# Optimization experiments

Measured on AMD Instinct MI355X. Metric: run time of the kernel, lower is better.

## Reference

```python
import jax, jax.numpy as jnp
import numpy as np
from jax import lax


def _box_filter(x, r):
    # depthwise (groups=ch) 2D box conv matching torch nf.conv2d(..., groups=ch)
    ch = x.shape[1]
    k = 2 * r + 1
    kernel = jnp.full((ch, 1, k, k), 1.0 / (k * k), dtype=x.dtype)
    return lax.conv_general_dilated(
        x, kernel,
        window_strides=(1, 1),
        padding=[(r, r), (r, r)],
        feature_group_count=ch,
        dimension_numbers=("NCHW", "OIHW", "NCHW"))


def setup_inputs() -> dict:
    key = jax.random.key(0)
    kx, ky = jax.random.split(key)
    B, C, H, W = 8, 3, 512, 512
    x = jax.random.uniform(kx, (B, C, H, W), dtype=jnp.float32)
    y = jax.random.uniform(ky, (B, C, H, W), dtype=jnp.float32)
    return {"x": x, "y": y, "r": 5}


def reference(x, y, r):
    eps = 0.01
    b, c, h, w = x.shape
    N = _box_filter(jnp.ones((1, 1, h, w), dtype=x.dtype), r)  # [1,1,H,W]
    mean_x = _box_filter(x, r) / N
    mean_y = _box_filter(y, r) / N
    cov_xy = _box_filter(x * y, r) / N - mean_x * mean_y
    var_x = _box_filter(x * x, r) / N - mean_x * mean_x
    A = cov_xy / (var_x + eps)
    bb = mean_y - A * mean_x
    mean_A = _box_filter(A, r) / N
    mean_b = _box_filter(bb, r) / N
    return mean_A * x + mean_b
```

## Files before the change

kernel.cpp:

```cpp
#include <hip/hip_runtime.h>


#define R    5
#define TX   64
#define TY   16
#define IMG  512
#define AROWS (TY + 2 * R)
#define ACOLS (TX + 2 * R)
#define XCOLS (TX + 4 * R)
#define V4STR 97
#define ABSTR 83
#define OFF_VAB 17280
#define SMEM_TOTAL (AROWS * V4STR * 16)

#define PB(c) ((c) + ((c) >> 3))

__device__ __forceinline__ float ccnt(int g) {
    int lo = max(g - R, 0), hi = min(g + R, IMG - 1);
    return (float)(hi - lo + 1);
}

__global__ __launch_bounds__(256, 4) void guided_fused(
        const float* __restrict__ x, const float* __restrict__ y,
        float* __restrict__ out) {
    __shared__ __align__(16) unsigned char smem[SMEM_TOTAL];
    float4 (*v4)[V4STR] = (float4(*)[V4STR])smem;
    float2 (*ab2)[ABSTR] = (float2(*)[ABSTR])smem;
    float2 (*vab)[ABSTR] = (float2(*)[ABSTR])(smem + OFF_VAB);

    const int plane = blockIdx.z;
    const int tx0 = blockIdx.x * TX;
    const int ty0 = blockIdx.y * TY;
    const int tid = threadIdx.x;
    const size_t pbase = (size_t)plane * IMG * IMG;
    const float* xp = x + pbase;
    const float* yp = y + pbase;
    const bool interior = (tx0 >= 2 * R) && (tx0 + TX + 2 * R - 1 < IMG) &&
                          (ty0 >= 2 * R) && (ty0 + TY + 2 * R - 1 < IMG);

    if (tid < 3 * XCOLS) {
        const int seg = tid / XCOLS;
        const int cc  = tid - seg * XCOLS;
        const int r0  = seg * 9;
        const int gx  = tx0 - 2 * R + cc;
        const int gy0 = ty0 - 2 * R + r0;

        float xv[19], yv[19];
        if (interior) {
            const float* xc = xp + (size_t)gy0 * IMG + gx;
            const float* yc = yp + (size_t)gy0 * IMG + gx;
#pragma unroll
            for (int j = 0; j < 19; ++j) {
                xv[j] = xc[(size_t)j * IMG];
                yv[j] = yc[(size_t)j * IMG];
            }
        } else {
            const bool xok = ((unsigned)gx < (unsigned)IMG);
#pragma unroll
            for (int j = 0; j < 19; ++j) {
                int gy = gy0 + j;
                bool ok = xok && ((unsigned)gy < (unsigned)IMG);
                size_t o = (size_t)gy * IMG + gx;
                xv[j] = ok ? xp[o] : 0.f;
                yv[j] = ok ? yp[o] : 0.f;
            }
        }
        float sx = 0.f, sy = 0.f, sxy = 0.f, sxx = 0.f;
#pragma unroll
        for (int j = 0; j < 11; ++j) {
            sx += xv[j]; sy += yv[j];
            sxy += xv[j] * yv[j]; sxx += xv[j] * xv[j];
        }
        v4[r0][PB(cc)] = make_float4(sx, sy, sxy, sxx);
#pragma unroll
        for (int s = 1; s < 9; ++s) {
            if (r0 + s < AROWS) {
                float xn = xv[s + 10], yn = yv[s + 10];
                float xo = xv[s - 1],  yo = yv[s - 1];
                sx  += xn - xo;
                sy  += yn - yo;
                sxy += xn * yn - xo * yo;
                sxx += xn * xn - xo * xo;
                v4[r0 + s][PB(cc)] = make_float4(sx, sy, sxy, sxx);
            }
        }
    }
    __syncthreads();

    int p2_r = 0, p2_c0 = 0, p2_nout = 0;
    float2 pres[10];
    if (tid < 8 * AROWS) {
        const int ch = tid / AROWS;
        const int r  = tid - ch * AROWS;
        const int c0 = 10 * ch;
        const int nout = min(10, ACOLS - c0);
        p2_r = r; p2_c0 = c0; p2_nout = nout;

        float4 ring[10];
#pragma unroll
        for (int d = 0; d < 10; ++d) ring[d] = v4[r][PB(c0 + d)];
        float sx = 0.f, sy = 0.f, sxy = 0.f, sxx = 0.f;
#pragma unroll
        for (int d = 0; d < 10; ++d) {
            sx += ring[d].x; sy += ring[d].y;
            sxy += ring[d].z; sxx += ring[d].w;
        }
        const int ay = ty0 - R + r;
        const float cy = ccnt(ay);
        const bool ayok = ((unsigned)ay < (unsigned)IMG);
#pragma unroll
        for (int i = 0; i < 10; ++i) {
            if (i < nout) {
                float4 lead = v4[r][PB(c0 + 10 + i)];
                sx += lead.x; sy += lead.y; sxy += lead.z; sxx += lead.w;
                if (i > 0) {
                    float4 o = ring[(i > 0) ? (i - 1) : 0];
                    sx -= o.x; sy -= o.y; sxy -= o.z; sxx -= o.w;
                }
                const int ac = c0 + i;
                const int ax = tx0 - R + ac;
                float A = 0.f, bb = 0.f;
                if (interior || (ayok && ((unsigned)ax < (unsigned)IMG))) {
                    float inv = interior ? (1.0f / 121.0f)
                                         : __builtin_amdgcn_rcpf(cy * ccnt(ax));
                    float mx = sx * inv, my = sy * inv;
                    float cov = sxy * inv - mx * my;
                    float var = sxx * inv - mx * mx;
                    A = cov * __builtin_amdgcn_rcpf(var + 0.01f);
                    bb = my - A * mx;
                }
                pres[i] = make_float2(A, bb);
            }
        }
    }
    __syncthreads();

    if (tid < 8 * AROWS) {
#pragma unroll
        for (int i = 0; i < 10; ++i) {
            if (i < p2_nout) ab2[p2_r][PB(p2_c0 + i)] = pres[i];
        }
    }
    __syncthreads();

    if (tid < 2 * ACOLS) {
        const int seg = (tid >= ACOLS) ? 1 : 0;
        const int ac = tid - seg * ACOLS;
        const int r0 = seg * 8;
        float2 ring[10];
#pragma unroll
        for (int d = 0; d < 10; ++d) ring[d] = ab2[r0 + d][PB(ac)];
        float sa = 0.f, sb = 0.f;
#pragma unroll
        for (int d = 0; d < 10; ++d) { sa += ring[d].x; sb += ring[d].y; }
#pragma unroll
        for (int s = 0; s < 8; ++s) {
            float2 lead = ab2[r0 + 10 + s][PB(ac)];
            sa += lead.x; sb += lead.y;
            if (s > 0) {
                float2 o = ring[(s > 0) ? (s - 1) : 0];
                sa -= o.x; sb -= o.y;
            }
            vab[r0 + s][PB(ac)] = make_float2(sa, sb);
        }
    }
    __syncthreads();

    {
        const int oy = tid >> 4;
        const int ch = tid & 15;
        const int c0 = 4 * ch;
        const int gy = ty0 + oy;
        float2 ring[10];
#pragma unroll
        for (int d = 0; d < 10; ++d) ring[d] = vab[oy][PB(c0 + d)];
        float sa = 0.f, sb = 0.f;
#pragma unroll
        for (int d = 0; d < 10; ++d) { sa += ring[d].x; sb += ring[d].y; }
        const float cy = ccnt(gy);
        const size_t obase = (size_t)gy * IMG + tx0 + c0;
        const float4 xv4 = *reinterpret_cast<const float4*>(&xp[obase]);
        const float xv[4] = {xv4.x, xv4.y, xv4.z, xv4.w};
        float res[4];
#pragma unroll
        for (int i = 0; i < 4; ++i) {
            float2 lead = vab[oy][PB(c0 + 10 + i)];
            sa += lead.x; sb += lead.y;
            if (i > 0) {
                float2 o = ring[(i > 0) ? (i - 1) : 0];
                sa -= o.x; sb -= o.y;
            }
            float inv = interior ? (1.0f / 121.0f)
                                 : __builtin_amdgcn_rcpf(cy * ccnt(tx0 + c0 + i));
            res[i] = (sa * inv) * xv[i] + (sb * inv);
        }
        *reinterpret_cast<float4*>(&out[pbase + obase]) =
            make_float4(res[0], res[1], res[2], res[3]);
    }
}

extern "C" void kernel_launch(void* const* d_in, const int* in_sizes, int n_in,
                              void* d_out, int out_size, void* d_ws, size_t ws_size,
                              hipStream_t stream) {
    const float* x = (const float*)d_in[0];
    const float* y = (const float*)d_in[1];
    float* out = (float*)d_out;

    const int planes = in_sizes[0] / (IMG * IMG);

    dim3 grid(IMG / TX, IMG / TY, planes);
    guided_fused<<<grid, 256, 0, stream>>>(x, y, out);
}
```

Measured before the change: 118.8 us.

## Rebalance horizontal passes into 8-column chunks and prefetch x before final pass

The horizontal box-sum pass now splits columns into 8-wide chunks aligned with the padding period, so shared-memory addresses become base plus constant offsets, and it uses 9 chunk threads per row instead of 8. The final output pass has 128 threads each produce 8 outputs, and the x values it needs are loaded from global memory earlier, overlapping that load with the ab2 write and the vertical pass. This aims to cut address arithmetic and hide global-load latency. In exchange, half the threads sit idle in the last pass and the per-thread serial work there doubles.

```diff
diff --git a/kernel.cpp b/kernel.cpp
--- a/kernel.cpp
+++ b/kernel.cpp
@@ -13,7 +13,8 @@
 #define OFF_VAB 17280
 #define SMEM_TOTAL (AROWS * V4STR * 16)
 
-#define PB(c) ((c) + ((c) >> 3))
+#define PB(c)   ((c) + ((c) >> 3))
+#define OFFD(d) ((d) + ((d) >> 3))
 
 __device__ __forceinline__ float ccnt(int g) {
     int lo = max(g - R, 0), hi = min(g + R, IMG - 1);
@@ -71,7 +72,8 @@
             sx += xv[j]; sy += yv[j];
             sxy += xv[j] * yv[j]; sxx += xv[j] * xv[j];
         }
-        v4[r0][PB(cc)] = make_float4(sx, sy, sxy, sxx);
+        float4* wp = &v4[r0][PB(cc)];
+        wp[0] = make_float4(sx, sy, sxy, sxx);
 #pragma unroll
         for (int s = 1; s < 9; ++s) {
             if (r0 + s < AROWS) {
@@ -81,24 +83,25 @@
                 sy  += yn - yo;
                 sxy += xn * yn - xo * yo;
                 sxx += xn * xn - xo * xo;
-                v4[r0 + s][PB(cc)] = make_float4(sx, sy, sxy, sxx);
-            }
-        }
-    }
-    __syncthreads();
-
-    int p2_r = 0, p2_c0 = 0, p2_nout = 0;
+                wp[(size_t)s * V4STR] = make_float4(sx, sy, sxy, sxx);
+            }
+        }
+    }
+    __syncthreads();
+
+    int p2_r = 0, p2_pb0 = 0, p2_nout = 0;
     float2 pres[10];
-    if (tid < 8 * AROWS) {
+    if (tid < 9 * AROWS) {
         const int ch = tid / AROWS;
         const int r  = tid - ch * AROWS;
-        const int c0 = 10 * ch;
-        const int nout = min(10, ACOLS - c0);
-        p2_r = r; p2_c0 = c0; p2_nout = nout;
-
+        const int c0 = 8 * ch;
+        const int nout = (ch == 8) ? 10 : 8;
+        p2_r = r; p2_pb0 = 9 * ch; p2_nout = nout;
+
+        const float4* bp = &v4[r][p2_pb0];
         float4 ring[10];
 #pragma unroll
-        for (int d = 0; d < 10; ++d) ring[d] = v4[r][PB(c0 + d)];
+        for (int d = 0; d < 10; ++d) ring[d] = bp[OFFD(d)];
         float sx = 0.f, sy = 0.f, sxy = 0.f, sxx = 0.f;
 #pragma unroll
         for (int d = 0; d < 10; ++d) {
@@ -111,10 +114,10 @@
 #pragma unroll
         for (int i = 0; i < 10; ++i) {
             if (i < nout) {
-                float4 lead = v4[r][PB(c0 + 10 + i)];
+                float4 lead = bp[OFFD(10 + i)];
                 sx += lead.x; sy += lead.y; sxy += lead.z; sxx += lead.w;
                 if (i > 0) {
-                    float4 o = ring[(i > 0) ? (i - 1) : 0];
+                    float4 o = ring[i - 1];
                     sx -= o.x; sy -= o.y; sxy -= o.z; sxx -= o.w;
                 }
                 const int ac = c0 + i;
@@ -135,10 +138,21 @@
     }
     __syncthreads();
 
-    if (tid < 8 * AROWS) {
+    float4 xpa = make_float4(0.f, 0.f, 0.f, 0.f), xpb = xpa;
+    size_t obase = 0;
+    if (tid < TY * 8) {
+        const int oy = tid >> 3;
+        const int ch = tid & 7;
+        obase = (size_t)(ty0 + oy) * IMG + tx0 + 8 * ch;
+        xpa = *reinterpret_cast<const float4*>(&xp[obase]);
+        xpb = *reinterpret_cast<const float4*>(&xp[obase + 4]);
+    }
+
+    if (tid < 9 * AROWS) {
+        float2* bw = &ab2[p2_r][p2_pb0];
 #pragma unroll
         for (int i = 0; i < 10; ++i) {
-            if (i < p2_nout) ab2[p2_r][PB(p2_c0 + i)] = pres[i];
+            if (i < p2_nout) bw[OFFD(i)] = pres[i];
         }
     }
     __syncthreads();
@@ -147,47 +161,49 @@
         const int seg = (tid >= ACOLS) ? 1 : 0;
         const int ac = tid - seg * ACOLS;
         const int r0 = seg * 8;
+        const float2* rp = &ab2[r0][PB(ac)];
+        float2* wp = &vab[r0][PB(ac)];
         float2 ring[10];
 #pragma unroll
-        for (int d = 0; d < 10; ++d) ring[d] = ab2[r0 + d][PB(ac)];
+        for (int d = 0; d < 10; ++d) ring[d] = rp[(size_t)d * ABSTR];
         float sa = 0.f, sb = 0.f;
 #pragma unroll
         for (int d = 0; d < 10; ++d) { sa += ring[d].x; sb += ring[d].y; }
 #pragma unroll
         for (int s = 0; s < 8; ++s) {
-            float2 lead = ab2[r0 + 10 + s][PB(ac)];
+            float2 lead = rp[(size_t)(10 + s) * ABSTR];
             sa += lead.x; sb += lead.y;
             if (s > 0) {
-                float2 o = ring[(s > 0) ? (s - 1) : 0];
+                float2 o = ring[s - 1];
                 sa -= o.x; sb -= o.y;
             }
-            vab[r0 + s][PB(ac)] = make_float2(sa, sb);
-        }
-    }
-    __syncthreads();
-
-    {
-        const int oy = tid >> 4;
-        const int ch = tid & 15;
-        const int c0 = 4 * ch;
+            wp[(size_t)s * ABSTR] = make_float2(sa, sb);
+        }
+    }
+    __syncthreads();
+
+    if (tid < TY * 8) {
+        const int oy = tid >> 3;
+        const int ch = tid & 7;
+        const int c0 = 8 * ch;
+        const float2* vb = &vab[oy][9 * ch];
+        float2 ring[10];
+#pragma unroll
+        for (int d = 0; d < 10; ++d) ring[d] = vb[OFFD(d)];
+        float sa = 0.f, sb = 0.f;
+#pragma unroll
+        for (int d = 0; d < 10; ++d) { sa += ring[d].x; sb += ring[d].y; }
         const int gy = ty0 + oy;
-        float2 ring[10];
-#pragma unroll
-        for (int d = 0; d < 10; ++d) ring[d] = vab[oy][PB(c0 + d)];
-        float sa = 0.f, sb = 0.f;
-#pragma unroll
-        for (int d = 0; d < 10; ++d) { sa += ring[d].x; sb += ring[d].y; }
         const float cy = ccnt(gy);
-        const size_t obase = (size_t)gy * IMG + tx0 + c0;
-        const float4 xv4 = *reinterpret_cast<const float4*>(&xp[obase]);
-        const float xv[4] = {xv4.x, xv4.y, xv4.z, xv4.w};
-        float res[4];
-#pragma unroll
-        for (int i = 0; i < 4; ++i) {
-            float2 lead = vab[oy][PB(c0 + 10 + i)];
+        const float xv[8] = {xpa.x, xpa.y, xpa.z, xpa.w,
+                             xpb.x, xpb.y, xpb.z, xpb.w};
+        float res[8];
+#pragma unroll
+        for (int i = 0; i < 8; ++i) {
+            float2 lead = vb[OFFD(10 + i)];
             sa += lead.x; sb += lead.y;
             if (i > 0) {
-                float2 o = ring[(i > 0) ? (i - 1) : 0];
+                float2 o = ring[i - 1];
                 sa -= o.x; sb -= o.y;
             }
             float inv = interior ? (1.0f / 121.0f)
@@ -196,6 +212,8 @@
         }
         *reinterpret_cast<float4*>(&out[pbase + obase]) =
             make_float4(res[0], res[1], res[2], res[3]);
+        *reinterpret_cast<float4*>(&out[pbase + obase + 4]) =
+            make_float4(res[4], res[5], res[6], res[7]);
     }
 }
 
```

New measurement: 117.7 us. No clear change (-0.9%).
